# Kernel optimization log

Measured on AMD Instinct MI355X. Metric: run time of the kernel, lower is better.

The kernel has to match this reference:

```python
import jax, jax.numpy as jnp
import numpy as np

HEADS = 16
LN_EPS = 1e-5


def _layernorm(x, w, b):
    mu = jnp.mean(x, axis=-1, keepdims=True)
    var = jnp.mean(jnp.square(x - mu), axis=-1, keepdims=True)
    return (x - mu) * jax.lax.rsqrt(var + LN_EPS) * w + b


def setup_inputs() -> dict:
    key = jax.random.key(0)
    ks = jax.random.split(key, 14)
    B, L, E, HID = 4, 4096, 1024, 4096
    s = 0.02
    return {
        "x": jax.random.normal(ks[0], (B, L, E), dtype=jnp.float32),
        "w_q": jax.random.normal(ks[1], (E, E), dtype=jnp.float32) * s,
        "w_k": jax.random.normal(ks[2], (E, E), dtype=jnp.float32) * s,
        "w_v": jax.random.normal(ks[3], (E, E), dtype=jnp.float32) * s,
        "w_o": jax.random.normal(ks[4], (E, E), dtype=jnp.float32) * s,
        "b_o": jnp.zeros((E,), dtype=jnp.float32),
        "ln1_w": jnp.ones((E,), dtype=jnp.float32),
        "ln1_b": jnp.zeros((E,), dtype=jnp.float32),
        "ln2_w": jnp.ones((E,), dtype=jnp.float32),
        "ln2_b": jnp.zeros((E,), dtype=jnp.float32),
        "w_ff1": jax.random.normal(ks[5], (E, HID), dtype=jnp.float32) * s,
        "b_ff1": jnp.zeros((HID,), dtype=jnp.float32),
        "w_ff2": jax.random.normal(ks[6], (HID, E), dtype=jnp.float32) * s,
        "b_ff2": jnp.zeros((E,), dtype=jnp.float32),
    }


def reference(x, w_q, w_k, w_v, w_o, b_o, ln1_w, ln1_b, ln2_w, ln2_b,
              w_ff1, b_ff1, w_ff2, b_ff2):
    N, L, E = x.shape
    H = HEADS
    D = E // H
    # projections -> (N, H, L, D) exactly as the torch view+permute
    q = (x @ w_q).reshape(N, L, H, D).transpose(0, 2, 1, 3)
    k = (x @ w_k).reshape(N, L, H, D).transpose(0, 2, 1, 3)
    v = (x @ w_v).reshape(N, L, H, D).transpose(0, 2, 1, 3)
    # Faithful to source: einsum subscripts applied to the PERMUTED tensors,
    # so 'q'/'k' bind to the heads axis and 'h','d' contract over (length, head_dim).
    # energy: (N, H, H)
    energy = jnp.einsum('nqhd,nkhd->nqk', q, k)
    attention = jax.nn.softmax(energy / (float(E) ** 0.5), axis=2)
    # 'k' and 'v' are independent sum indices -> out[n,q,h,d] = (sum_k att) * (sum_v v)
    out = jnp.einsum('nqk,nvhd->nqhd', attention, v)  # (N, H, L, D)
    out = out.reshape(N, L, H * D)  # row-major flatten, same as torch .reshape
    attn_out = out @ w_o + b_o
    # residual + LayerNorm (dropout is identity in eval)
    h1 = _layernorm(attn_out + x, ln1_w, ln1_b)
    ff = jax.nn.relu(h1 @ w_ff1 + b_ff1) @ w_ff2 + b_ff2
    return _layernorm(ff + h1, ln2_w, ln2_b)
```

## Files before the change

kernel.cpp:

```cpp
#include <hip/hip_runtime.h>
#include <stdint.h>
#include <stddef.h>

typedef __bf16 bf16_t;
typedef __bf16 bf16x8 __attribute__((ext_vector_type(8)));
typedef __bf16 bf16x4 __attribute__((ext_vector_type(4)));
typedef float f32x4 __attribute__((ext_vector_type(4)));

#define E_DIM 1024
#define HID_DIM 4096
#define NROWS 16384

__device__ __forceinline__ void async16(const bf16_t* g, void* l) {
    __builtin_amdgcn_global_load_lds(
        (const __attribute__((address_space(1))) void*)g,
        (__attribute__((address_space(3))) void*)l,
        16, 0, 0);
}

__global__ void detect_dtype(const unsigned int* __restrict__ ln1_w_raw, int* __restrict__ flag) {
    if (threadIdx.x == 0) {
        *flag = (ln1_w_raw[0] == 0x3F800000u) ? 0 : 1;
    }
}

__device__ __forceinline__ float load_in(const void* p, size_t idx, int isb) {
    if (isb) return (float)((const bf16_t*)p)[idx];
    return ((const float*)p)[idx];
}

struct VecArgs {
    const void* p[7];
    float* o[7];
    int n[7];
};

__global__ __launch_bounds__(256) void convert_vecs(VecArgs a, const int* __restrict__ dflag) {
    int isb = *dflag;
    int seg = blockIdx.y;
    int i = blockIdx.x * 256 + threadIdx.x;
    if (i < a.n[seg]) a.o[seg][i] = load_in(a.p[seg], (size_t)i, isb);
}

__global__ __launch_bounds__(256) void convert_x(const void* __restrict__ in, bf16_t* __restrict__ out,
                                                 const int* __restrict__ dflag) {
    int isb = *dflag;
    size_t i = ((size_t)blockIdx.x * 256 + threadIdx.x) * 8;
    if (isb) {
        *(bf16x8*)(out + i) = *((const bf16x8*)((const bf16_t*)in + i));
    } else {
        const float* f = (const float*)in + i;
        bf16x8 v;
#pragma unroll
        for (int j = 0; j < 8; j++) v[j] = (bf16_t)f[j];
        *(bf16x8*)(out + i) = v;
    }
}

__global__ void transpose_to_bf16(const void* __restrict__ in, bf16_t* __restrict__ out,
                                  int R, int C, const int* __restrict__ dflag) {
    int isb = *dflag;
    __shared__ bf16_t tile[32][33];
    int c0 = blockIdx.x * 32, r0 = blockIdx.y * 32;
    int tx = threadIdx.x, ty = threadIdx.y;
#pragma unroll
    for (int i = 0; i < 32; i += 8)
        tile[ty + i][tx] = (bf16_t)load_in(in, (size_t)(r0 + ty + i) * C + (c0 + tx), isb);
    __syncthreads();
#pragma unroll
    for (int i = 0; i < 32; i += 8)
        out[(size_t)(c0 + ty + i) * R + (r0 + tx)] = tile[tx][ty + i];
}

__global__ void fold_wv(const void* __restrict__ w_v, bf16_t* __restrict__ w_vs_t,
                        const int* __restrict__ dflag) {
    int isb = *dflag;
    int d = threadIdx.x;
    int e = blockIdx.x;
    float s = 0.f;
#pragma unroll
    for (int i = 0; i < 16; i++)
        s += load_in(w_v, (size_t)e * 1024 + i * 64 + d, isb);
    w_vs_t[((size_t)d << 10) + e] = (bf16_t)s;
}

template <int BM, int BN, int SWZ_G, bool RELU, bool OUT_BF16, bool HAS_BIAS>
__global__ __launch_bounds__(256) void gemm_bt(const bf16_t* __restrict__ A,
                                               const bf16_t* __restrict__ Bt,
                                               const float* __restrict__ bias,
                                               void* __restrict__ Cv,
                                               int M, int N, int K) {
    constexpr int BK = 64;
    constexpr int WM = BM / 2;
    constexpr int WN = BN / 2;
    constexpr int TM = WM / 16;
    constexpr int TN = WN / 16;
    __shared__ __align__(16) bf16_t As[BM][BK];
    __shared__ __align__(16) bf16_t Bs[BN][BK];

    const int tid = threadIdx.x;
    const int lane = tid & 63;
    const int wid = tid >> 6;
    const int wr = wid >> 1, wc = wid & 1;
    const int lm = lane & 15, quad = lane >> 4;
    const int lm7 = lm & 7;

    int bx = blockIdx.x, by = blockIdx.y;
    if (SWZ_G > 0) {
        const int flat = by * gridDim.x + bx;
        const int S = SWZ_G * gridDim.x;
        const int g = flat / S, r = flat % S;
        bx = r / SWZ_G;
        by = g * SWZ_G + (r % SWZ_G);
    }
    const int bm = by * BM, bn = bx * BN;

    const int rsub = lane >> 3;
    const int csub = ((lane & 7) ^ rsub) << 3;

    f32x4 acc[TM][TN];
#pragma unroll
    for (int i = 0; i < TM; i++)
#pragma unroll
        for (int j = 0; j < TN; j++) acc[i][j] = (f32x4){0.f, 0.f, 0.f, 0.f};

    const bf16_t* Ap = A + (size_t)bm * K + csub;
    const bf16_t* Bp = Bt + (size_t)bn * K + csub;

    for (int k0 = 0; k0 < K; k0 += BK) {
#pragma unroll
        for (int cc = 0; cc < BM / 32; cc++) {
            const int c = cc * 4 + wid;
            async16(Ap + (size_t)(c * 8 + rsub) * K + k0, (char*)&As[0][0] + c * 1024);
        }
#pragma unroll
        for (int cc = 0; cc < BN / 32; cc++) {
            const int c = cc * 4 + wid;
            async16(Bp + (size_t)(c * 8 + rsub) * K + k0, (char*)&Bs[0][0] + c * 1024);
        }
        __syncthreads();

#pragma unroll
        for (int kk = 0; kk < 2; kk++) {
            bf16x8 af[TM], bfr[TN];
#pragma unroll
            for (int i = 0; i < TM; i++) {
                const int row = wr * WM + i * 16 + lm;
                const int pb = ((kk * 4 + quad) ^ lm7) << 3;
                af[i] = *(const bf16x8*)(&As[row][pb]);
            }
#pragma unroll
            for (int j = 0; j < TN; j++) {
                const int row = wc * WN + j * 16 + lm;
                const int pb = ((kk * 4 + quad) ^ lm7) << 3;
                bfr[j] = *(const bf16x8*)(&Bs[row][pb]);
            }
#pragma unroll
            for (int i = 0; i < TM; i++)
#pragma unroll
                for (int j = 0; j < TN; j++)
                    acc[i][j] = __builtin_amdgcn_mfma_f32_16x16x32_bf16(af[i], bfr[j], acc[i][j], 0, 0, 0);
        }
        __syncthreads();
    }

    const int gm0 = bm + wr * WM, gn0 = bn + wc * WN;
#pragma unroll
    for (int i = 0; i < TM; i++) {
#pragma unroll
        for (int j = 0; j < TN; j++) {
            const int col = gn0 + j * 16 + lm;
            float bv = HAS_BIAS ? bias[col] : 0.f;
#pragma unroll
            for (int r = 0; r < 4; r++) {
                const int row = gm0 + i * 16 + quad * 4 + r;
                float v = acc[i][j][r] + bv;
                if (RELU) v = fmaxf(v, 0.f);
                if (OUT_BF16)
                    ((bf16_t*)Cv)[(size_t)row * N + col] = (bf16_t)v;
                else
                    ((float*)Cv)[(size_t)row * N + col] = v;
            }
        }
    }
}

template <int SWZ_G, bool RELU, bool OUT_BF16, bool HAS_BIAS>
__global__ __launch_bounds__(512, 2) void gemm256(const bf16_t* __restrict__ A,
                                                  const bf16_t* __restrict__ Bt,
                                                  const float* __restrict__ bias,
                                                  void* __restrict__ Cv,
                                                  int M, int N, int K) {
    constexpr int BK = 64;
    __shared__ __align__(16) bf16_t As[2][256][BK];
    __shared__ __align__(16) bf16_t Bs[2][256][BK];

    const int tid = threadIdx.x;
    const int lane = tid & 63;
    const int wid = tid >> 6;
    const int wr = wid >> 2;
    const int wc = wid & 3;
    const int lm = lane & 15, quad = lane >> 4;
    const int lm7 = lm & 7;
    const int rsub = lane >> 3;
    const int csub = ((lane & 7) ^ rsub) << 3;

    int bx = blockIdx.x, by = blockIdx.y;
    if (SWZ_G > 0) {
        const int flat = by * gridDim.x + bx;
        const int S = SWZ_G * gridDim.x;
        const int g = flat / S, r = flat % S;
        bx = r / SWZ_G;
        by = g * SWZ_G + (r % SWZ_G);
    }
    const int bm = by * 256, bn = bx * 256;

    const bf16_t* Ap = A + (size_t)bm * K + csub;
    const bf16_t* Bp = Bt + (size_t)bn * K + csub;
    const int c0 = wid * 2;

#define STAGE_A(b, h, kt) do { \
        const size_t ko = (size_t)(kt) * BK; \
        async16(Ap + (size_t)((h) * 128 + c0 * 8 + rsub) * K + ko, \
                (char*)(&As[(b)][0][0]) + (h) * 16384 + c0 * 1024); \
        async16(Ap + (size_t)((h) * 128 + (c0 + 1) * 8 + rsub) * K + ko, \
                (char*)(&As[(b)][0][0]) + (h) * 16384 + (c0 + 1) * 1024); \
    } while (0)
#define STAGE_B(b, h, kt) do { \
        const size_t ko = (size_t)(kt) * BK; \
        async16(Bp + (size_t)((h) * 128 + c0 * 8 + rsub) * K + ko, \
                (char*)(&Bs[(b)][0][0]) + (h) * 16384 + c0 * 1024); \
        async16(Bp + (size_t)((h) * 128 + (c0 + 1) * 8 + rsub) * K + ko, \
                (char*)(&Bs[(b)][0][0]) + (h) * 16384 + (c0 + 1) * 1024); \
    } while (0)

    f32x4 acc[8][4];
#pragma unroll
    for (int i = 0; i < 8; i++)
#pragma unroll
        for (int j = 0; j < 4; j++) acc[i][j] = (f32x4){0.f, 0.f, 0.f, 0.f};

    auto ldA = [&](int b, int im, int kk) -> bf16x8 {
        const int row = wr * 128 + im * 16 + lm;
        const int pb = ((kk * 4 + quad) ^ lm7) << 3;
        return *(const bf16x8*)(&As[b][row][pb]);
    };
    auto ldB = [&](int b, int jn, int kk) -> bf16x8 {
        const int row = wc * 64 + jn * 16 + lm;
        const int pb = ((kk * 4 + quad) ^ lm7) << 3;
        return *(const bf16x8*)(&Bs[b][row][pb]);
    };

    const int nt = K / BK;

    STAGE_A(0, 0, 0); STAGE_A(0, 1, 0);
    STAGE_B(0, 0, 0); STAGE_B(0, 1, 0);
    if (nt > 1) {
        STAGE_B(1, 0, 1); STAGE_B(1, 1, 1);
        asm volatile("s_waitcnt vmcnt(4)" ::: "memory");
    } else {
        asm volatile("s_waitcnt vmcnt(0)" ::: "memory");
    }
    __builtin_amdgcn_s_barrier();

    bf16x8 af[4][2], bfr[4][2];
    for (int t = 0; t < nt; ++t) {
        const int cur = t & 1, nxt = cur ^ 1;

#pragma unroll
        for (int im = 0; im < 4; ++im)
#pragma unroll
            for (int kk = 0; kk < 2; ++kk) af[im][kk] = ldA(cur, im, kk);
#pragma unroll
        for (int jn = 0; jn < 2; ++jn)
#pragma unroll
            for (int kk = 0; kk < 2; ++kk) bfr[jn][kk] = ldB(cur, jn, kk);
        if (t + 1 < nt) STAGE_A(nxt, 0, t + 1);
        __builtin_amdgcn_s_barrier();
        asm volatile("s_waitcnt lgkmcnt(0)" ::: "memory");
        __builtin_amdgcn_sched_barrier(0);
        __builtin_amdgcn_s_setprio(1);
#pragma unroll
        for (int kk = 0; kk < 2; ++kk)
#pragma unroll
            for (int i = 0; i < 4; ++i)
#pragma unroll
                for (int j = 0; j < 2; ++j)
                    acc[i][j] = __builtin_amdgcn_mfma_f32_16x16x32_bf16(af[i][kk], bfr[j][kk], acc[i][j], 0, 0, 0);
        __builtin_amdgcn_s_setprio(0);
        __builtin_amdgcn_s_barrier();

#pragma unroll
        for (int jn = 2; jn < 4; ++jn)
#pragma unroll
            for (int kk = 0; kk < 2; ++kk) bfr[jn][kk] = ldB(cur, jn, kk);
        if (t + 1 < nt) STAGE_A(nxt, 1, t + 1);
        __builtin_amdgcn_s_barrier();
        asm volatile("s_waitcnt lgkmcnt(0)" ::: "memory");
        __builtin_amdgcn_sched_barrier(0);
        __builtin_amdgcn_s_setprio(1);
#pragma unroll
        for (int kk = 0; kk < 2; ++kk)
#pragma unroll
            for (int i = 0; i < 4; ++i)
#pragma unroll
                for (int j = 2; j < 4; ++j)
                    acc[i][j] = __builtin_amdgcn_mfma_f32_16x16x32_bf16(af[i][kk], bfr[j][kk], acc[i][j], 0, 0, 0);
        __builtin_amdgcn_s_setprio(0);
        __builtin_amdgcn_s_barrier();

#pragma unroll
        for (int im = 0; im < 4; ++im)
#pragma unroll
            for (int kk = 0; kk < 2; ++kk) af[im][kk] = ldA(cur, im + 4, kk);
        if (t + 2 < nt) STAGE_B(cur, 0, t + 2);
        __builtin_amdgcn_s_barrier();
        asm volatile("s_waitcnt lgkmcnt(0)" ::: "memory");
        __builtin_amdgcn_sched_barrier(0);
        __builtin_amdgcn_s_setprio(1);
#pragma unroll
        for (int kk = 0; kk < 2; ++kk)
#pragma unroll
            for (int i = 0; i < 4; ++i)
#pragma unroll
                for (int j = 2; j < 4; ++j)
                    acc[4 + i][j] = __builtin_amdgcn_mfma_f32_16x16x32_bf16(af[i][kk], bfr[j][kk], acc[4 + i][j], 0, 0, 0);
        __builtin_amdgcn_s_setprio(0);
        __builtin_amdgcn_s_barrier();

        if (t + 2 < nt) STAGE_B(cur, 1, t + 2);
        __builtin_amdgcn_s_setprio(1);
#pragma unroll
        for (int kk = 0; kk < 2; ++kk)
#pragma unroll
            for (int i = 0; i < 4; ++i)
#pragma unroll
                for (int j = 0; j < 2; ++j)
                    acc[4 + i][j] = __builtin_amdgcn_mfma_f32_16x16x32_bf16(af[i][kk], bfr[j][kk], acc[4 + i][j], 0, 0, 0);
        __builtin_amdgcn_s_setprio(0);
        if (t + 2 < nt) {
            asm volatile("s_waitcnt vmcnt(4)" ::: "memory");
        } else {
            asm volatile("s_waitcnt vmcnt(0)" ::: "memory");
        }
        __builtin_amdgcn_s_barrier();
    }
#undef STAGE_A
#undef STAGE_B

    const int gm0 = bm + wr * 128, gn0 = bn + wc * 64;
#pragma unroll
    for (int i = 0; i < 8; i++) {
#pragma unroll
        for (int j = 0; j < 4; j++) {
            const int col = gn0 + j * 16 + lm;
            float bv = HAS_BIAS ? bias[col] : 0.f;
#pragma unroll
            for (int r = 0; r < 4; r++) {
                const int row = gm0 + i * 16 + quad * 4 + r;
                float v = acc[i][j][r] + bv;
                if (RELU) v = fmaxf(v, 0.f);
                if (OUT_BF16)
                    ((bf16_t*)Cv)[(size_t)row * N + col] = (bf16_t)v;
                else
                    ((float*)Cv)[(size_t)row * N + col] = v;
            }
        }
    }
}

__device__ __forceinline__ void block_reduce2(float& s, float& s2, float* red, int tid) {
#pragma unroll
    for (int o = 32; o > 0; o >>= 1) {
        s += __shfl_down(s, o, 64);
        s2 += __shfl_down(s2, o, 64);
    }
    const int wid = tid >> 6;
    if ((tid & 63) == 0) { red[wid] = s; red[4 + wid] = s2; }
    __syncthreads();
    s = red[0] + red[1] + red[2] + red[3];
    s2 = red[4] + red[5] + red[6] + red[7];
}

__global__ __launch_bounds__(256) void ln1_fused(const float* __restrict__ attn,
                                                 const bf16_t* __restrict__ xbf,
                                                 const float* __restrict__ w,
                                                 const float* __restrict__ b,
                                                 bf16_t* __restrict__ h1) {
    const int row = blockIdx.x;
    const int n = row >> 12;
    const int lp = row & 4095;
    const float* arow = attn + (((size_t)(n << 8) + (lp & 255)) << 10);
    const bf16_t* xrow = xbf + ((size_t)row << 10);
    const int tid = threadIdx.x;
    const int c4 = tid << 2;
    __shared__ float red[8];
    f32x4 a = *(const f32x4*)(arow + c4);
    bf16x4 xv = *(const bf16x4*)(xrow + c4);
    float v[4];
    float s = 0.f, s2 = 0.f;
#pragma unroll
    for (int u = 0; u < 4; u++) {
        float val = a[u] + (float)xv[u];
        v[u] = val; s += val; s2 += val * val;
    }
    block_reduce2(s, s2, red, tid);
    const float mu = s * (1.f / 1024.f);
    const float var = s2 * (1.f / 1024.f) - mu * mu;
    const float rstd = rsqrtf(var + 1e-5f);
    f32x4 wv = *(const f32x4*)(w + c4);
    f32x4 bv = *(const f32x4*)(b + c4);
    bf16x4 hv;
#pragma unroll
    for (int u = 0; u < 4; u++)
        hv[u] = (bf16_t)((v[u] - mu) * rstd * wv[u] + bv[u]);
    *(bf16x4*)(h1 + ((size_t)row << 10) + c4) = hv;
}

__global__ __launch_bounds__(256) void ln2_fused(const bf16_t* __restrict__ ff,
                                                 const bf16_t* __restrict__ h1,
                                                 const float* __restrict__ w,
                                                 const float* __restrict__ b,
                                                 void* __restrict__ outp,
                                                 const int* __restrict__ dflag,
                                                 int row0) {
    const int isb = *dflag;
    const int row = blockIdx.x;
    const int tid = threadIdx.x;
    const int c4 = tid << 2;
    __shared__ float red[8];
    bf16x4 fv = *(const bf16x4*)(ff + ((size_t)row << 10) + c4);
    bf16x4 hv = *(const bf16x4*)(h1 + ((size_t)row << 10) + c4);
    float v[4];
    float s = 0.f, s2 = 0.f;
#pragma unroll
    for (int u = 0; u < 4; u++) {
        float val = (float)fv[u] + (float)hv[u];
        v[u] = val; s += val; s2 += val * val;
    }
    block_reduce2(s, s2, red, tid);
    const float mu = s * (1.f / 1024.f);
    const float var = s2 * (1.f / 1024.f) - mu * mu;
    const float rstd = rsqrtf(var + 1e-5f);
    f32x4 wv = *(const f32x4*)(w + c4);
    f32x4 bv = *(const f32x4*)(b + c4);
    const size_t base = ((size_t)(row0 + row) << 10) + c4;
    if (isb) {
        bf16x4 ov;
#pragma unroll
        for (int u = 0; u < 4; u++) ov[u] = (bf16_t)((v[u] - mu) * rstd * wv[u] + bv[u]);
        *(bf16x4*)((bf16_t*)outp + base) = ov;
    } else {
        f32x4 ov;
#pragma unroll
        for (int u = 0; u < 4; u++) ov[u] = (v[u] - mu) * rstd * wv[u] + bv[u];
        *(f32x4*)((float*)outp + base) = ov;
    }
}

extern "C" void kernel_launch(void* const* d_in, const int* in_sizes, int n_in,
                              void* d_out, int out_size, void* d_ws, size_t ws_size,
                              hipStream_t stream) {
    char* ws = (char*)d_ws;
    const size_t MB = 1u << 20;

    int*    dflag   = (int*)ws;
    float*  vec0    = (float*)(ws + 4096);
    float*  vec_b_o   = vec0 + 0 * 4096;
    float*  vec_bff1  = vec0 + 1 * 4096;
    float*  vec_bff2  = vec0 + 2 * 4096;
    float*  vec_ln1w  = vec0 + 3 * 4096;
    float*  vec_ln1b  = vec0 + 4 * 4096;
    float*  vec_ln2w  = vec0 + 5 * 4096;
    float*  vec_ln2b  = vec0 + 6 * 4096;
    bf16_t* w_vs_t  = (bf16_t*)(ws + 256 * 1024);
    bf16_t* w_o_t   = (bf16_t*)(ws + 1 * MB);
    bf16_t* w_ff1_t = (bf16_t*)(ws + 3 * MB);
    bf16_t* w_ff2_t = (bf16_t*)(ws + 11 * MB);
    bf16_t* vsum    = (bf16_t*)(ws + 19 * MB);
    float*  attn    = (float*)(ws + 21 * MB);
    bf16_t* xbf     = (bf16_t*)(ws + 25 * MB);
    bf16_t* h1      = (bf16_t*)(ws + 57 * MB);
    bf16_t* hidden  = (bf16_t*)(ws + 89 * MB);

    int chunk;
    if (ws_size >= 250 * MB)      chunk = 16384;
    else if (ws_size >= 170 * MB) chunk = 8192;
    else                          chunk = 4096;
    bf16_t* ffbuf = (bf16_t*)(ws + 89 * MB + (size_t)chunk * HID_DIM * sizeof(bf16_t));

    detect_dtype<<<1, 64, 0, stream>>>((const unsigned int*)d_in[6], dflag);

    VecArgs va;
    va.p[0] = d_in[5];  va.o[0] = vec_b_o;  va.n[0] = 1024;
    va.p[1] = d_in[11]; va.o[1] = vec_bff1; va.n[1] = 4096;
    va.p[2] = d_in[13]; va.o[2] = vec_bff2; va.n[2] = 1024;
    va.p[3] = d_in[6];  va.o[3] = vec_ln1w; va.n[3] = 1024;
    va.p[4] = d_in[7];  va.o[4] = vec_ln1b; va.n[4] = 1024;
    va.p[5] = d_in[8];  va.o[5] = vec_ln2w; va.n[5] = 1024;
    va.p[6] = d_in[9];  va.o[6] = vec_ln2b; va.n[6] = 1024;
    convert_vecs<<<dim3(16, 7), 256, 0, stream>>>(va, dflag);

    convert_x<<<8192, 256, 0, stream>>>(d_in[0], xbf, dflag);

    transpose_to_bf16<<<dim3(32, 32),  dim3(32, 8), 0, stream>>>(d_in[4],  w_o_t,   1024, 1024, dflag);
    transpose_to_bf16<<<dim3(128, 32), dim3(32, 8), 0, stream>>>(d_in[10], w_ff1_t, 1024, 4096, dflag);
    transpose_to_bf16<<<dim3(32, 128), dim3(32, 8), 0, stream>>>(d_in[12], w_ff2_t, 4096, 1024, dflag);
    fold_wv<<<1024, 64, 0, stream>>>(d_in[3], w_vs_t, dflag);

    gemm_bt<128, 64, 0, false, true, false><<<dim3(1, 128), 256, 0, stream>>>(
        xbf, w_vs_t, nullptr, vsum, NROWS, 64, E_DIM);

    gemm_bt<128, 128, 0, false, false, true><<<dim3(8, 8), 256, 0, stream>>>(
        vsum, w_o_t, vec_b_o, attn, 1024, 1024, 1024);

    ln1_fused<<<NROWS, 256, 0, stream>>>(attn, xbf, vec_ln1w, vec_ln1b, h1);

    for (int r0 = 0; r0 < NROWS; r0 += chunk) {
        const bf16_t* h1c = h1 + (size_t)r0 * E_DIM;
        gemm256<16, true, true, true><<<dim3(HID_DIM / 256, chunk / 256), 512, 0, stream>>>(
            h1c, w_ff1_t, vec_bff1, hidden, chunk, HID_DIM, E_DIM);
        gemm256<16, false, true, true><<<dim3(E_DIM / 256, chunk / 256), 512, 0, stream>>>(
            hidden, w_ff2_t, vec_bff2, ffbuf, chunk, E_DIM, HID_DIM);
        ln2_fused<<<chunk, 256, 0, stream>>>(ffbuf, h1c, vec_ln2w, vec_ln2b, d_out, dflag, r0);
    }
}
```

Before: 505.2 us.

## Restructure gemm256 main loop to prefetch A and B two tiles ahead

```diff
diff --git a/kernel.cpp b/kernel.cpp
--- a/kernel.cpp
+++ b/kernel.cpp
@@ -233,6 +233,11 @@
         async16(Bp + (size_t)((h) * 128 + (c0 + 1) * 8 + rsub) * K + ko, \
                 (char*)(&Bs[(b)][0][0]) + (h) * 16384 + (c0 + 1) * 1024); \
     } while (0)
+#define FENCE_BARRIER() do { \
+        asm volatile("" ::: "memory"); \
+        __builtin_amdgcn_s_barrier(); \
+        asm volatile("" ::: "memory"); \
+    } while (0)
 
     f32x4 acc[8][4];
 #pragma unroll
@@ -256,97 +261,86 @@
     STAGE_A(0, 0, 0); STAGE_A(0, 1, 0);
     STAGE_B(0, 0, 0); STAGE_B(0, 1, 0);
     if (nt > 1) {
+        STAGE_A(1, 0, 1); STAGE_A(1, 1, 1);
         STAGE_B(1, 0, 1); STAGE_B(1, 1, 1);
-        asm volatile("s_waitcnt vmcnt(4)" ::: "memory");
+        asm volatile("s_waitcnt vmcnt(8)" ::: "memory");
     } else {
         asm volatile("s_waitcnt vmcnt(0)" ::: "memory");
     }
     __builtin_amdgcn_s_barrier();
-
-    bf16x8 af[4][2], bfr[4][2];
+    asm volatile("" ::: "memory");
+
+    bf16x8 afA[4], afB[4], b01[2][2], b23[2][2];
     for (int t = 0; t < nt; ++t) {
-        const int cur = t & 1, nxt = cur ^ 1;
-
-#pragma unroll
-        for (int im = 0; im < 4; ++im)
-#pragma unroll
-            for (int kk = 0; kk < 2; ++kk) af[im][kk] = ldA(cur, im, kk);
-#pragma unroll
-        for (int jn = 0; jn < 2; ++jn)
-#pragma unroll
-            for (int kk = 0; kk < 2; ++kk) bfr[jn][kk] = ldB(cur, jn, kk);
-        if (t + 1 < nt) STAGE_A(nxt, 0, t + 1);
-        __builtin_amdgcn_s_barrier();
-        asm volatile("s_waitcnt lgkmcnt(0)" ::: "memory");
-        __builtin_amdgcn_sched_barrier(0);
+        const int cur = t & 1;
+        const bool pf = (t + 2 < nt);
+
+#pragma unroll
+        for (int i = 0; i < 4; ++i) afA[i] = ldA(cur, i, 0);
+#pragma unroll
+        for (int j = 0; j < 2; ++j) b01[j][0] = ldB(cur, j, 0);
+#pragma unroll
+        for (int i = 0; i < 4; ++i) afB[i] = ldA(cur, i, 1);
+#pragma unroll
+        for (int j = 0; j < 2; ++j) b01[j][1] = ldB(cur, j, 1);
+#pragma unroll
+        for (int j = 0; j < 2; ++j) b23[j][0] = ldB(cur, 2 + j, 0);
+#pragma unroll
+        for (int j = 0; j < 2; ++j) b23[j][1] = ldB(cur, 2 + j, 1);
         __builtin_amdgcn_s_setprio(1);
 #pragma unroll
-        for (int kk = 0; kk < 2; ++kk)
-#pragma unroll
-            for (int i = 0; i < 4; ++i)
-#pragma unroll
-                for (int j = 0; j < 2; ++j)
-                    acc[i][j] = __builtin_amdgcn_mfma_f32_16x16x32_bf16(af[i][kk], bfr[j][kk], acc[i][j], 0, 0, 0);
+        for (int i = 0; i < 4; ++i)
+#pragma unroll
+            for (int j = 0; j < 2; ++j) {
+                acc[i][j] = __builtin_amdgcn_mfma_f32_16x16x32_bf16(afA[i], b01[j][0], acc[i][j], 0, 0, 0);
+                acc[i][j] = __builtin_amdgcn_mfma_f32_16x16x32_bf16(afB[i], b01[j][1], acc[i][j], 0, 0, 0);
+            }
+#pragma unroll
+        for (int i = 0; i < 4; ++i)
+#pragma unroll
+            for (int j = 0; j < 2; ++j) {
+                acc[i][2 + j] = __builtin_amdgcn_mfma_f32_16x16x32_bf16(afA[i], b23[j][0], acc[i][2 + j], 0, 0, 0);
+                acc[i][2 + j] = __builtin_amdgcn_mfma_f32_16x16x32_bf16(afB[i], b23[j][1], acc[i][2 + j], 0, 0, 0);
+            }
         __builtin_amdgcn_s_setprio(0);
-        __builtin_amdgcn_s_barrier();
-
-#pragma unroll
-        for (int jn = 2; jn < 4; ++jn)
-#pragma unroll
-            for (int kk = 0; kk < 2; ++kk) bfr[jn][kk] = ldB(cur, jn, kk);
-        if (t + 1 < nt) STAGE_A(nxt, 1, t + 1);
-        __builtin_amdgcn_s_barrier();
-        asm volatile("s_waitcnt lgkmcnt(0)" ::: "memory");
-        __builtin_amdgcn_sched_barrier(0);
+#pragma unroll
+        for (int i = 0; i < 4; ++i) afA[i] = ldA(cur, 4 + i, 0);
+        FENCE_BARRIER();
+
+#pragma unroll
+        for (int i = 0; i < 4; ++i) afB[i] = ldA(cur, 4 + i, 1);
+        if (pf) { STAGE_B(cur, 0, t + 2); STAGE_B(cur, 1, t + 2); }
         __builtin_amdgcn_s_setprio(1);
 #pragma unroll
-        for (int kk = 0; kk < 2; ++kk)
-#pragma unroll
-            for (int i = 0; i < 4; ++i)
-#pragma unroll
-                for (int j = 2; j < 4; ++j)
-                    acc[i][j] = __builtin_amdgcn_mfma_f32_16x16x32_bf16(af[i][kk], bfr[j][kk], acc[i][j], 0, 0, 0);
+        for (int i = 0; i < 4; ++i)
+#pragma unroll
+            for (int j = 0; j < 2; ++j) {
+                acc[4 + i][2 + j] = __builtin_amdgcn_mfma_f32_16x16x32_bf16(afA[i], b23[j][0], acc[4 + i][2 + j], 0, 0, 0);
+                acc[4 + i][2 + j] = __builtin_amdgcn_mfma_f32_16x16x32_bf16(afB[i], b23[j][1], acc[4 + i][2 + j], 0, 0, 0);
+            }
         __builtin_amdgcn_s_setprio(0);
-        __builtin_amdgcn_s_barrier();
-
-#pragma unroll
-        for (int im = 0; im < 4; ++im)
-#pragma unroll
-            for (int kk = 0; kk < 2; ++kk) af[im][kk] = ldA(cur, im + 4, kk);
-        if (t + 2 < nt) STAGE_B(cur, 0, t + 2);
-        __builtin_amdgcn_s_barrier();
-        asm volatile("s_waitcnt lgkmcnt(0)" ::: "memory");
-        __builtin_amdgcn_sched_barrier(0);
+        FENCE_BARRIER();
+
+        if (pf) { STAGE_A(cur, 0, t + 2); STAGE_A(cur, 1, t + 2); }
         __builtin_amdgcn_s_setprio(1);
 #pragma unroll
-        for (int kk = 0; kk < 2; ++kk)
-#pragma unroll
-            for (int i = 0; i < 4; ++i)
-#pragma unroll
-                for (int j = 2; j < 4; ++j)
-                    acc[4 + i][j] = __builtin_amdgcn_mfma_f32_16x16x32_bf16(af[i][kk], bfr[j][kk], acc[4 + i][j], 0, 0, 0);
+        for (int i = 0; i < 4; ++i)
+#pragma unroll
+            for (int j = 0; j < 2; ++j) {
+                acc[4 + i][j] = __builtin_amdgcn_mfma_f32_16x16x32_bf16(afA[i], b01[j][0], acc[4 + i][j], 0, 0, 0);
+                acc[4 + i][j] = __builtin_amdgcn_mfma_f32_16x16x32_bf16(afB[i], b01[j][1], acc[4 + i][j], 0, 0, 0);
+            }
         __builtin_amdgcn_s_setprio(0);
-        __builtin_amdgcn_s_barrier();
-
-        if (t + 2 < nt) STAGE_B(cur, 1, t + 2);
-        __builtin_amdgcn_s_setprio(1);
-#pragma unroll
-        for (int kk = 0; kk < 2; ++kk)
-#pragma unroll
-            for (int i = 0; i < 4; ++i)
-#pragma unroll
-                for (int j = 0; j < 2; ++j)
-                    acc[4 + i][j] = __builtin_amdgcn_mfma_f32_16x16x32_bf16(af[i][kk], bfr[j][kk], acc[4 + i][j], 0, 0, 0);
-        __builtin_amdgcn_s_setprio(0);
-        if (t + 2 < nt) {
-            asm volatile("s_waitcnt vmcnt(4)" ::: "memory");
+        if (pf) {
+            asm volatile("s_waitcnt vmcnt(8)" ::: "memory");
         } else {
             asm volatile("s_waitcnt vmcnt(0)" ::: "memory");
         }
-        __builtin_amdgcn_s_barrier();
+        FENCE_BARRIER();
     }
 #undef STAGE_A
 #undef STAGE_B
+#undef FENCE_BARRIER
 
     const int gm0 = bm + wr * 128, gn0 = bn + wc * 64;
 #pragma unroll
@@ -508,7 +502,7 @@
     transpose_to_bf16<<<dim3(32, 128), dim3(32, 8), 0, stream>>>(d_in[12], w_ff2_t, 4096, 1024, dflag);
     fold_wv<<<1024, 64, 0, stream>>>(d_in[3], w_vs_t, dflag);
 
-    gemm_bt<128, 64, 0, false, true, false><<<dim3(1, 128), 256, 0, stream>>>(
+    gemm_bt<64, 64, 0, false, true, false><<<dim3(1, 256), 256, 0, stream>>>(
         xbf, w_vs_t, nullptr, vsum, NROWS, 64, E_DIM);
 
     gemm_bt<128, 128, 0, false, false, true><<<dim3(8, 8), 256, 0, stream>>>(
```

After: 549.8 us. +8.8%, slower.
